# Optimization experiments

Hardware: AMD Instinct MI355X
Metric: run time of the kernel (lower is better)

Reference implementation:

```python
import jax, jax.numpy as jnp
import numpy as np

C_S = 1024
H = 16
M = 1  # num_vector_messages
B, S = 2, 1024
SQRT3 = 3.0 ** 0.5
LN_EPS = 1e-5


def setup_inputs() -> dict:
    key = jax.random.key(0)
    ks = jax.random.split(key, 8)
    s = jax.random.normal(ks[0], (B, S, C_S), dtype=jnp.float32)
    # random proper-ish frames: orthonormalize random 3x3 via QR
    A = jax.random.normal(ks[1], (B, S, 3, 3), dtype=jnp.float32)
    rot, _ = jnp.linalg.qr(A)
    trans = jax.random.normal(ks[2], (B, S, 3), dtype=jnp.float32)
    affine_mask = jnp.ones((B, S), dtype=bool)
    sequence_id = jax.random.randint(ks[3], (B, S), 0, 4, dtype=jnp.int32)
    chain_id = jax.random.randint(ks[4], (B, S), 0, 4, dtype=jnp.int32)
    dim_proj = 4 * H * 3 + H * 3 * M
    ln_w = jnp.ones((C_S,), dtype=jnp.float32)
    w_proj = jax.random.normal(ks[5], (dim_proj, C_S), dtype=jnp.float32) / np.sqrt(C_S)
    w_out = jax.random.normal(ks[6], (C_S, H * 3 * M), dtype=jnp.float32) / np.sqrt(H * 3 * M)
    dist_scale = jnp.zeros((H,), dtype=jnp.float32)
    rot_scale = jnp.zeros((H,), dtype=jnp.float32)
    return {"s": s, "rot": rot, "trans": trans, "ln_w": ln_w, "w_proj": w_proj,
            "w_out": w_out, "dist_scale": dist_scale, "rot_scale": rot_scale,
            "affine_mask": affine_mask, "sequence_id": sequence_id, "chain_id": chain_id}


def reference(s, rot, trans, ln_w, w_proj, w_out, dist_scale, rot_scale,
              affine_mask, sequence_id, chain_id):
    b, n, c = s.shape
    h, m = H, M
    NEG = jnp.finfo(s.dtype).min
    # attention bias: 1.0 for same-sequence pairs, -inf for invalid frames / cross-chain
    seq_eq = (sequence_id[:, :, None] == sequence_id[:, None, :]).astype(s.dtype)
    bias = seq_eq[:, None]  # [b,1,s,s]
    bias = jnp.where(affine_mask[:, None, None, :], bias, NEG)
    chain_diff = chain_id[:, :, None] != chain_id[:, None, :]
    bias = jnp.where(chain_diff[:, None], NEG, bias)
    # LayerNorm (no bias)
    mu = jnp.mean(s, axis=-1, keepdims=True)
    var = jnp.var(s, axis=-1, keepdims=True)
    ns = (s - mu) / jnp.sqrt(var + LN_EPS) * ln_w
    p = jnp.einsum('bsc,dc->bsd', ns, w_proj)
    n_rot = h * 2 * 3 + h * 3 * m
    vec_rot = p[..., :n_rot].reshape(b, n, 2 * h + h * m, 3)
    vec_dist = p[..., n_rot:].reshape(b, n, 2 * h, 3)
    # rotate into global frame; dist vectors also translated
    rot_vecs = jnp.einsum('bsij,bshj->bshi', rot, vec_rot)
    q_rot, k_rot, value = rot_vecs[:, :, :h], rot_vecs[:, :, h:2 * h], rot_vecs[:, :, 2 * h:]
    dist_vecs = jnp.einsum('bsij,bshj->bshi', rot, vec_dist) + trans[:, :, None, :]
    q_dist, k_dist = dist_vecs[:, :, :h], dist_vecs[:, :, h:]
    # distance term [b,h,q,k]
    qd = q_dist.transpose(0, 2, 1, 3)  # b h s 3
    kd = k_dist.transpose(0, 2, 1, 3)
    diff = qd[:, :, :, None, :] - kd[:, :, None, :, :]
    distance_term = jnp.sqrt(jnp.sum(diff * diff, axis=-1)) / SQRT3
    rotation_term = jnp.einsum('bqhd,bkhd->bhqk', q_rot, k_rot) / SQRT3
    dw = jax.nn.softplus(dist_scale)[None, :, None, None]
    rw = jax.nn.softplus(rot_scale)[None, :, None, None]
    attn = rotation_term * rw - distance_term * dw + bias
    attn = jax.nn.softmax(attn, axis=-1)
    # value: b s (h m) 3 -> b h s (m 3)
    v = value.reshape(b, n, h, m, 3).transpose(0, 2, 1, 3, 4).reshape(b, h, n, m * 3)
    out = jnp.einsum('bhqk,bhkd->bhqd', attn, v)
    out = out.reshape(b, h, n, m, 3).transpose(0, 2, 1, 3, 4).reshape(b, n, h * m, 3)
    out = jnp.einsum('bsji,bshj->bshi', rot, out)  # inverse rotation R^T
    out = out.reshape(b, n, h * m * 3)
    out = jnp.where(affine_mask[..., None], out, 0.0)
    return jnp.einsum('bsd,cd->bsc', out, w_out)
```

## Files before the change

### kernel.cpp

```cpp
#include <hip/hip_runtime.h>
#include <math.h>

#define NB 2
#define NS 1024
#define NC 1024
#define NH 16
#define DIMP 240
#define KSPLIT 16

constexpr float INV_SQRT3 = 0.57735026919f;

__global__ __launch_bounds__(256) void pre_kernel(const float* __restrict__ s,
                                                  const float* __restrict__ lnw,
                                                  float* __restrict__ ns,
                                                  const float* __restrict__ wp,
                                                  float* __restrict__ wt) {
    __shared__ float sh[64 * 61];
    int tid = threadIdx.x;
    if (blockIdx.x < NB * NS) {
        int row = blockIdx.x;
        const float4* sp = (const float4*)(s + (size_t)row * NC);
        float4 v = sp[tid];
        float sum = v.x + v.y + v.z + v.w;
        float sq  = v.x*v.x + v.y*v.y + v.z*v.z + v.w*v.w;
        #pragma unroll
        for (int off = 32; off; off >>= 1) {
            sum += __shfl_down(sum, off);
            sq  += __shfl_down(sq, off);
        }
        float* s1 = sh; float* s2 = sh + 4;
        int wave = tid >> 6;
        if ((tid & 63) == 0) { s1[wave] = sum; s2[wave] = sq; }
        __syncthreads();
        float tot   = s1[0] + s1[1] + s1[2] + s1[3];
        float totsq = s2[0] + s2[1] + s2[2] + s2[3];
        float mu  = tot * (1.0f / NC);
        float var = totsq * (1.0f / NC) - mu * mu;
        float rstd = rsqrtf(var + 1e-5f);
        float4 w = ((const float4*)lnw)[tid];
        float4 o;
        o.x = (v.x - mu) * rstd * w.x;
        o.y = (v.y - mu) * rstd * w.y;
        o.z = (v.z - mu) * rstd * w.z;
        o.w = (v.w - mu) * rstd * w.w;
        ((float4*)(ns + (size_t)row * NC))[tid] = o;
    } else {
        int bx = blockIdx.x - NB * NS;
        int k0 = (bx & 15) * 64;
        int d0 = (bx >> 4) * 60;
        float (*T)[61] = (float (*)[61])sh;
        #pragma unroll
        for (int i = 0; i < 15; i++) {
            int idx = i * 256 + tid;
            int dd = idx >> 6, kk = idx & 63;
            T[kk][dd] = wp[(size_t)(d0 + dd) * NC + k0 + kk];
        }
        __syncthreads();
        #pragma unroll
        for (int i = 0; i < 15; i++) {
            int idx = i * 256 + tid;
            int kk = idx / 60, dd = idx % 60;
            wt[(size_t)(k0 + kk) * DIMP + d0 + dd] = T[kk][dd];
        }
    }
}

__global__ __launch_bounds__(256) void proj_kernel(const float* __restrict__ ns,
                                                   const float* __restrict__ wt,
                                                   float* __restrict__ pp,
                                                   int use_atomic) {
    int tid = threadIdx.x;
    int wave = tid >> 6, lane = tid & 63;
    int row0 = blockIdx.x * 32;
    int ky = blockIdx.y;
    int k0 = ky * 64;

    __shared__ float A[32][64];
    #pragma unroll
    for (int i = 0; i < 2; i++) {
        int idx = tid + i * 256;
        int r = idx >> 4, c4 = idx & 15;
        *(float4*)&A[r][c4 * 4] = *(const float4*)(ns + (size_t)(row0 + r) * NC + k0 + c4 * 4);
    }
    __syncthreads();

    int wr0 = wave * 8;
    int c0 = lane * 4;
    bool active = c0 < DIMP;
    int c0m = active ? c0 : (DIMP - 4);
    const float* wb = wt + (size_t)k0 * DIMP + c0m;

    float acc[8][4];
    #pragma unroll
    for (int r = 0; r < 8; r++)
        #pragma unroll
        for (int c = 0; c < 4; c++) acc[r][c] = 0.0f;

    float4 wa[4], wx[4];
    #pragma unroll
    for (int j = 0; j < 4; j++) wa[j] = *(const float4*)(wb + (size_t)j * DIMP);

    for (int g = 0; g < 16; g += 2) {
        #pragma unroll
        for (int j = 0; j < 4; j++)
            wx[j] = *(const float4*)(wb + (size_t)((g + 1) * 4 + j) * DIMP);
        #pragma unroll
        for (int r = 0; r < 8; r++) {
            float4 a4 = *(const float4*)&A[wr0 + r][g * 4];
            #pragma unroll
            for (int c = 0; c < 4; c++) {
                float* ac = &acc[r][c];
                *ac = fmaf(a4.x, ((const float*)&wa[0])[c], *ac);
                *ac = fmaf(a4.y, ((const float*)&wa[1])[c], *ac);
                *ac = fmaf(a4.z, ((const float*)&wa[2])[c], *ac);
                *ac = fmaf(a4.w, ((const float*)&wa[3])[c], *ac);
            }
        }
        int kn2 = (g + 2 < 16) ? (g + 2) * 4 : 0;
        #pragma unroll
        for (int j = 0; j < 4; j++)
            wa[j] = *(const float4*)(wb + (size_t)(kn2 + j) * DIMP);
        #pragma unroll
        for (int r = 0; r < 8; r++) {
            float4 a4 = *(const float4*)&A[wr0 + r][(g + 1) * 4];
            #pragma unroll
            for (int c = 0; c < 4; c++) {
                float* ac = &acc[r][c];
                *ac = fmaf(a4.x, ((const float*)&wx[0])[c], *ac);
                *ac = fmaf(a4.y, ((const float*)&wx[1])[c], *ac);
                *ac = fmaf(a4.z, ((const float*)&wx[2])[c], *ac);
                *ac = fmaf(a4.w, ((const float*)&wx[3])[c], *ac);
            }
        }
    }
    if (active) {
        if (use_atomic) {
            #pragma unroll
            for (int r = 0; r < 8; r++)
                #pragma unroll
                for (int c = 0; c < 4; c++)
                    atomicAdd(&pp[(size_t)(row0 + wr0 + r) * DIMP + c0 + c], acc[r][c]);
        } else {
            float* dst = pp + (size_t)ky * (NB * NS * DIMP);
            #pragma unroll
            for (int r = 0; r < 8; r++)
                *(float4*)(dst + (size_t)(row0 + wr0 + r) * DIMP + c0) =
                    make_float4(acc[r][0], acc[r][1], acc[r][2], acc[r][3]);
        }
    }
}

__global__ __launch_bounds__(256) void build_kernel(const float* __restrict__ pp, int nred,
                                                    const float* __restrict__ rot,
                                                    const float* __restrict__ trans,
                                                    const float* __restrict__ dist_scale,
                                                    const float* __restrict__ rot_scale,
                                                    const int* __restrict__ seq,
                                                    const int* __restrict__ chain,
                                                    const int* __restrict__ amask,
                                                    float4* __restrict__ qrb,
                                                    float4* __restrict__ qdb,
                                                    float4* __restrict__ kp) {
    int gid = blockIdx.x * 256 + threadIdx.x;
    if (gid >= NB * NS * 80) return;
    int j  = gid % 80;
    int bs = gid / 80;
    int b  = bs >> 10;
    int si = bs & 1023;
    int off = (j < 48) ? 3 * j : 144 + 3 * (j - 48);
    float vx = 0.0f, vy = 0.0f, vz = 0.0f;
    for (int ky = 0; ky < nred; ky++) {
        const float* pr = pp + (size_t)ky * (NB * NS * DIMP) + (size_t)bs * DIMP + off;
        vx += pr[0]; vy += pr[1]; vz += pr[2];
    }
    const float* R = rot + (size_t)bs * 9;
    float ox = R[0] * vx + R[1] * vy + R[2] * vz;
    float oy = R[3] * vx + R[4] * vy + R[5] * vz;
    float oz = R[6] * vx + R[7] * vy + R[8] * vz;
    if (j >= 48) {
        ox += trans[(size_t)bs * 3 + 0];
        oy += trans[(size_t)bs * 3 + 1];
        oz += trans[(size_t)bs * 3 + 2];
    }
    if (j < 16) {
        float sc = log1pf(__expf(rot_scale[j])) * INV_SQRT3;
        qrb[(size_t)(b * NH + j) * NS + si] = make_float4(ox * sc, oy * sc, oz * sc, 0.0f);
    } else if (j < 32) {
        int h = j - 16;
        float ck = (float)chain[bs] + 1000.0f * (float)(1 - amask[bs]);
        kp[((size_t)(b * NH + h) * NS + si) * 3 + 0] = make_float4(ox, oy, oz, ck);
    } else if (j < 48) {
        int h = j - 32;
        kp[((size_t)(b * NH + h) * NS + si) * 3 + 2] = make_float4(ox, oy, oz, 0.0f);
    } else if (j < 64) {
        int h = j - 48;
        float sc = log1pf(__expf(dist_scale[h])) * INV_SQRT3;
        qdb[(size_t)(b * NH + h) * NS + si] = make_float4(ox * sc, oy * sc, oz * sc, 0.0f);
    } else {
        int h = j - 64;
        float sc = log1pf(__expf(dist_scale[h])) * INV_SQRT3;
        kp[((size_t)(b * NH + h) * NS + si) * 3 + 1] =
            make_float4(ox * sc, oy * sc, oz * sc, (float)seq[bs]);
    }
}

__global__ __launch_bounds__(256) void attn_kernel(
    const float4* __restrict__ qrb, const float4* __restrict__ qdb,
    const float4* __restrict__ kp,
    const float* __restrict__ rot,
    float* __restrict__ small) {
    int wid  = blockIdx.x * 4 + (threadIdx.x >> 6);
    int lane = threadIdx.x & 63;
    int qg = wid & 255;
    int h  = (wid >> 8) & 15;
    int b  = wid >> 12;
    int base = (b * NH + h) * NS;
    int q0 = qg * 4;
    const float4* kb = kp + (size_t)base * 3;

    float qrx[4], qry[4], qrz[4], qdx[4], qdy[4], qdz[4], cq[4], sq[4];
    #pragma unroll
    for (int t = 0; t < 4; t++) {
        float4 a = qrb[base + q0 + t];
        float4 d = qdb[base + q0 + t];
        qrx[t] = a.x; qry[t] = a.y; qrz[t] = a.z;
        qdx[t] = d.x; qdy[t] = d.y; qdz[t] = d.z;
        cq[t] = kb[(size_t)(q0 + t) * 3 + 0].w;
        sq[t] = kb[(size_t)(q0 + t) * 3 + 1].w;
    }
    float l[4] = {0, 0, 0, 0}, ax[4] = {0, 0, 0, 0}, ay[4] = {0, 0, 0, 0}, az[4] = {0, 0, 0, 0};

    for (int k = lane; k < NS; k += 64) {
        float4 f0 = kb[(size_t)k * 3 + 0];
        float4 f1 = kb[(size_t)k * 3 + 1];
        float4 f2 = kb[(size_t)k * 3 + 2];
        #pragma unroll
        for (int t = 0; t < 4; t++) {
            float rt = fmaf(qrx[t], f0.x, fmaf(qry[t], f0.y, qrz[t] * f0.z));
            float dx = qdx[t] - f1.x, dy = qdy[t] - f1.y, dz = qdz[t] - f1.z;
            float d2 = fmaf(dx, dx, fmaf(dy, dy, dz * dz));
            float dist = sqrtf(d2);
            float dc = f0.w - cq[t];
            float arg = fmaf(-100.0f, fabsf(dc), rt - dist) +
                        ((f1.w == sq[t]) ? -15.0f : -16.0f);
            float pw = __expf(arg);
            l[t] += pw;
            ax[t] = fmaf(pw, f2.x, ax[t]);
            ay[t] = fmaf(pw, f2.y, ay[t]);
            az[t] = fmaf(pw, f2.z, az[t]);
        }
    }
    #pragma unroll
    for (int t = 0; t < 4; t++) {
        #pragma unroll
        for (int off = 32; off; off >>= 1) {
            l[t]  += __shfl_xor(l[t], off);
            ax[t] += __shfl_xor(ax[t], off);
            ay[t] += __shfl_xor(ay[t], off);
            az[t] += __shfl_xor(az[t], off);
        }
    }
    if (lane == 0) {
        #pragma unroll
        for (int t = 0; t < 4; t++) {
            int q = q0 + t;
            float inv = 1.0f / l[t];
            float ox = ax[t] * inv, oy = ay[t] * inv, oz = az[t] * inv;
            const float* R = rot + (size_t)(b * NS + q) * 9;
            float wx = R[0] * ox + R[3] * oy + R[6] * oz;
            float wy = R[1] * ox + R[4] * oy + R[7] * oz;
            float wz = R[2] * ox + R[5] * oy + R[8] * oz;
            if (cq[t] >= 500.0f) { wx = 0; wy = 0; wz = 0; }
            float* o = small + (size_t)(b * NS + q) * 48 + h * 3;
            o[0] = wx; o[1] = wy; o[2] = wz;
        }
    }
}

__global__ __launch_bounds__(256) void outgemm_kernel(const float* __restrict__ small,
                                                      const float* __restrict__ wout,
                                                      float* __restrict__ out) {
    int c  = blockIdx.y * 256 + threadIdx.x;
    int r0 = blockIdx.x * 16;
    __shared__ float sm[16][48];
    for (int i = threadIdx.x; i < 16 * 48; i += 256)
        sm[i / 48][i % 48] = small[(size_t)(r0 + i / 48) * 48 + i % 48];
    __syncthreads();
    float w[48];
    #pragma unroll
    for (int d = 0; d < 48; d += 4) {
        float4 t = *(const float4*)(wout + (size_t)c * 48 + d);
        w[d] = t.x; w[d + 1] = t.y; w[d + 2] = t.z; w[d + 3] = t.w;
    }
    #pragma unroll 4
    for (int r = 0; r < 16; r++) {
        float acc = 0.0f;
        #pragma unroll
        for (int d = 0; d < 48; d++) acc = fmaf(w[d], sm[r][d], acc);
        out[(size_t)(r0 + r) * NC + c] = acc;
    }
}

extern "C" void kernel_launch(void* const* d_in, const int* in_sizes, int n_in,
                              void* d_out, int out_size, void* d_ws, size_t ws_size,
                              hipStream_t stream) {
    const float* s     = (const float*)d_in[0];
    const float* rot   = (const float*)d_in[1];
    const float* trans = (const float*)d_in[2];
    const float* lnw   = (const float*)d_in[3];
    const float* wproj = (const float*)d_in[4];
    const float* wout  = (const float*)d_in[5];
    const float* dsc   = (const float*)d_in[6];
    const float* rsc   = (const float*)d_in[7];
    const int* amask   = (const int*)d_in[8];
    const int* seq     = (const int*)d_in[9];
    const int* chain   = (const int*)d_in[10];
    float* out = (float*)d_out;

    float* ns = (float*)d_ws;
    float4* qrb = (float4*)(ns + (size_t)NB * NS * NC);
    float4* qdb = qrb + (size_t)NB * NH * NS;
    float4* kpk = qdb + (size_t)NB * NH * NS;
    float* small = (float*)(kpk + (size_t)3 * NB * NH * NS);
    float* pp = small + (size_t)NB * NS * 48;
    float* wt = (float*)qrb;

    size_t need = ((char*)(pp + (size_t)KSPLIT * NB * NS * DIMP)) - (char*)d_ws;
    int use_atomic = (ws_size < need) ? 1 : 0;

    pre_kernel<<<NB * NS + 64, 256, 0, stream>>>(s, lnw, ns, wproj, wt);
    if (use_atomic) {
        hipMemsetAsync(pp, 0, (size_t)NB * NS * DIMP * sizeof(float), stream);
        proj_kernel<<<dim3(64, KSPLIT), 256, 0, stream>>>(ns, wt, pp, 1);
        build_kernel<<<(NB * NS * 80 + 255) / 256, 256, 0, stream>>>(pp, 1, rot, trans, dsc, rsc,
                                                                     seq, chain, amask, qrb, qdb, kpk);
    } else {
        proj_kernel<<<dim3(64, KSPLIT), 256, 0, stream>>>(ns, wt, pp, 0);
        build_kernel<<<(NB * NS * 80 + 255) / 256, 256, 0, stream>>>(pp, KSPLIT, rot, trans, dsc, rsc,
                                                                     seq, chain, amask, qrb, qdb, kpk);
    }
    attn_kernel<<<NB * NH * NS / 16, 256, 0, stream>>>(qrb, qdb, kpk, rot, small);
    outgemm_kernel<<<dim3(NB * NS / 16, 4), 256, 0, stream>>>(small, wout, out);
}
```

Before: 156.1 us.

## Stage keys in LDS and raise queries per wave to eight

The attention kernel now loads all 1024 key/dist/value float4 triples for one (batch, head) into shared memory once per block. Each of the four waves then handles eight queries instead of four, so the grid shrinks to 1024 blocks of 32 queries. This cuts repeated global/L2 key reads and amortizes each key load over more queries. In exchange it uses 48KB of LDS per block, which limits occupancy, and doubles the accumulator registers per thread.

```diff
diff --git a/kernel.cpp b/kernel.cpp
--- a/kernel.cpp
+++ b/kernel.cpp
@@ -209,33 +209,47 @@
     const float4* __restrict__ kp,
     const float* __restrict__ rot,
     float* __restrict__ small) {
-    int wid  = blockIdx.x * 4 + (threadIdx.x >> 6);
-    int lane = threadIdx.x & 63;
-    int qg = wid & 255;
-    int h  = (wid >> 8) & 15;
-    int b  = wid >> 12;
-    int base = (b * NH + h) * NS;
-    int q0 = qg * 4;
+    __shared__ float4 krS[NS];
+    __shared__ float4 kdS[NS];
+    __shared__ float4 vvS[NS];
+    int tid  = threadIdx.x;
+    int wave = tid >> 6, lane = tid & 63;
+    int bh = blockIdx.x >> 5;
+    int qc = blockIdx.x & 31;
+    int b  = bh >> 4;
+    int base = bh * NS;
+    int q0 = qc * 32 + wave * 8;
     const float4* kb = kp + (size_t)base * 3;
 
-    float qrx[4], qry[4], qrz[4], qdx[4], qdy[4], qdz[4], cq[4], sq[4];
-    #pragma unroll
-    for (int t = 0; t < 4; t++) {
+    for (int i = tid; i < NS; i += 256) {
+        krS[i] = kb[(size_t)i * 3 + 0];
+        kdS[i] = kb[(size_t)i * 3 + 1];
+        vvS[i] = kb[(size_t)i * 3 + 2];
+    }
+    __syncthreads();
+
+    float qrx[8], qry[8], qrz[8], qdx[8], qdy[8], qdz[8], cq[8], sq[8];
+    #pragma unroll
+    for (int t = 0; t < 8; t++) {
         float4 a = qrb[base + q0 + t];
         float4 d = qdb[base + q0 + t];
         qrx[t] = a.x; qry[t] = a.y; qrz[t] = a.z;
         qdx[t] = d.x; qdy[t] = d.y; qdz[t] = d.z;
-        cq[t] = kb[(size_t)(q0 + t) * 3 + 0].w;
-        sq[t] = kb[(size_t)(q0 + t) * 3 + 1].w;
-    }
-    float l[4] = {0, 0, 0, 0}, ax[4] = {0, 0, 0, 0}, ay[4] = {0, 0, 0, 0}, az[4] = {0, 0, 0, 0};
-
-    for (int k = lane; k < NS; k += 64) {
-        float4 f0 = kb[(size_t)k * 3 + 0];
-        float4 f1 = kb[(size_t)k * 3 + 1];
-        float4 f2 = kb[(size_t)k * 3 + 2];
-        #pragma unroll
-        for (int t = 0; t < 4; t++) {
+        cq[t] = krS[q0 + t].w;
+        sq[t] = kdS[q0 + t].w;
+    }
+    float l[8], ax[8], ay[8], az[8];
+    #pragma unroll
+    for (int t = 0; t < 8; t++) { l[t] = 0; ax[t] = 0; ay[t] = 0; az[t] = 0; }
+
+    #pragma unroll 2
+    for (int ki = 0; ki < 16; ki++) {
+        int k = ki * 64 + lane;
+        float4 f0 = krS[k];
+        float4 f1 = kdS[k];
+        float4 f2 = vvS[k];
+        #pragma unroll
+        for (int t = 0; t < 8; t++) {
             float rt = fmaf(qrx[t], f0.x, fmaf(qry[t], f0.y, qrz[t] * f0.z));
             float dx = qdx[t] - f1.x, dy = qdy[t] - f1.y, dz = qdz[t] - f1.z;
             float d2 = fmaf(dx, dx, fmaf(dy, dy, dz * dz));
@@ -251,7 +265,7 @@
         }
     }
     #pragma unroll
-    for (int t = 0; t < 4; t++) {
+    for (int t = 0; t < 8; t++) {
         #pragma unroll
         for (int off = 32; off; off >>= 1) {
             l[t]  += __shfl_xor(l[t], off);
@@ -262,7 +276,7 @@
     }
     if (lane == 0) {
         #pragma unroll
-        for (int t = 0; t < 4; t++) {
+        for (int t = 0; t < 8; t++) {
             int q = q0 + t;
             float inv = 1.0f / l[t];
             float ox = ax[t] * inv, oy = ay[t] * inv, oz = az[t] * inv;
@@ -271,6 +285,7 @@
             float wy = R[1] * ox + R[4] * oy + R[7] * oz;
             float wz = R[2] * ox + R[5] * oy + R[8] * oz;
             if (cq[t] >= 500.0f) { wx = 0; wy = 0; wz = 0; }
+            int h = bh & 15;
             float* o = small + (size_t)(b * NS + q) * 48 + h * 3;
             o[0] = wx; o[1] = wy; o[2] = wz;
         }
@@ -339,6 +354,6 @@
         build_kernel<<<(NB * NS * 80 + 255) / 256, 256, 0, stream>>>(pp, KSPLIT, rot, trans, dsc, rsc,
                                                                      seq, chain, amask, qrb, qdb, kpk);
     }
-    attn_kernel<<<NB * NH * NS / 16, 256, 0, stream>>>(qrb, qdb, kpk, rot, small);
+    attn_kernel<<<NB * NH * (NS / 32), 256, 0, stream>>>(qrb, qdb, kpk, rot, small);
     outgemm_kernel<<<dim3(NB * NS / 16, 4), 256, 0, stream>>>(small, wout, out);
 }
```

Result: no change. 158.6 us (+1.6%).

## Split attention over key chunks with shared-memory key tiles and a reduction kernel

Applied to the files above, without the earlier changes.

The attention kernel now gives one query per thread and splits the key dimension into 16 chunks of 64 keys. Each block stages its chunk in shared memory and writes partial sums (weighted value and normaliser) to a workspace. A new finalize kernel adds the partials, normalises, applies the inverse rotation and the mask. This removes the per-query cross-lane shuffle reductions and the repeated global key loads, at the cost of an extra launch and extra partial-sum traffic. The exponentials have no max-subtraction, which is safe only because the logits are bounded.

```diff
diff --git a/kernel.cpp b/kernel.cpp
--- a/kernel.cpp
+++ b/kernel.cpp
@@ -7,6 +7,7 @@
 #define NH 16
 #define DIMP 240
 #define KSPLIT 16
+#define AKH 16
 
 constexpr float INV_SQRT3 = 0.57735026919f;
 
@@ -207,74 +208,67 @@
 __global__ __launch_bounds__(256) void attn_kernel(
     const float4* __restrict__ qrb, const float4* __restrict__ qdb,
     const float4* __restrict__ kp,
-    const float* __restrict__ rot,
-    float* __restrict__ small) {
-    int wid  = blockIdx.x * 4 + (threadIdx.x >> 6);
-    int lane = threadIdx.x & 63;
-    int qg = wid & 255;
-    int h  = (wid >> 8) & 15;
-    int b  = wid >> 12;
-    int base = (b * NH + h) * NS;
-    int q0 = qg * 4;
+    float4* __restrict__ pacc) {
+    __shared__ float4 kS[192];
+    int bx = blockIdx.x;
+    int ks = bx & (AKH - 1), qc = (bx >> 4) & 3, bh = bx >> 6;
+    int tid = threadIdx.x;
+    int q = qc * 256 + tid;
+    int base = bh * NS;
     const float4* kb = kp + (size_t)base * 3;
 
-    float qrx[4], qry[4], qrz[4], qdx[4], qdy[4], qdz[4], cq[4], sq[4];
-    #pragma unroll
-    for (int t = 0; t < 4; t++) {
-        float4 a = qrb[base + q0 + t];
-        float4 d = qdb[base + q0 + t];
-        qrx[t] = a.x; qry[t] = a.y; qrz[t] = a.z;
-        qdx[t] = d.x; qdy[t] = d.y; qdz[t] = d.z;
-        cq[t] = kb[(size_t)(q0 + t) * 3 + 0].w;
-        sq[t] = kb[(size_t)(q0 + t) * 3 + 1].w;
-    }
-    float l[4] = {0, 0, 0, 0}, ax[4] = {0, 0, 0, 0}, ay[4] = {0, 0, 0, 0}, az[4] = {0, 0, 0, 0};
-
-    for (int k = lane; k < NS; k += 64) {
-        float4 f0 = kb[(size_t)k * 3 + 0];
-        float4 f1 = kb[(size_t)k * 3 + 1];
-        float4 f2 = kb[(size_t)k * 3 + 2];
-        #pragma unroll
-        for (int t = 0; t < 4; t++) {
-            float rt = fmaf(qrx[t], f0.x, fmaf(qry[t], f0.y, qrz[t] * f0.z));
-            float dx = qdx[t] - f1.x, dy = qdy[t] - f1.y, dz = qdz[t] - f1.z;
-            float d2 = fmaf(dx, dx, fmaf(dy, dy, dz * dz));
-            float dist = sqrtf(d2);
-            float dc = f0.w - cq[t];
-            float arg = fmaf(-100.0f, fabsf(dc), rt - dist) +
-                        ((f1.w == sq[t]) ? -15.0f : -16.0f);
-            float pw = __expf(arg);
-            l[t] += pw;
-            ax[t] = fmaf(pw, f2.x, ax[t]);
-            ay[t] = fmaf(pw, f2.y, ay[t]);
-            az[t] = fmaf(pw, f2.z, az[t]);
-        }
-    }
-    #pragma unroll
-    for (int t = 0; t < 4; t++) {
-        #pragma unroll
-        for (int off = 32; off; off >>= 1) {
-            l[t]  += __shfl_xor(l[t], off);
-            ax[t] += __shfl_xor(ax[t], off);
-            ay[t] += __shfl_xor(ay[t], off);
-            az[t] += __shfl_xor(az[t], off);
-        }
-    }
-    if (lane == 0) {
-        #pragma unroll
-        for (int t = 0; t < 4; t++) {
-            int q = q0 + t;
-            float inv = 1.0f / l[t];
-            float ox = ax[t] * inv, oy = ay[t] * inv, oz = az[t] * inv;
-            const float* R = rot + (size_t)(b * NS + q) * 9;
-            float wx = R[0] * ox + R[3] * oy + R[6] * oz;
-            float wy = R[1] * ox + R[4] * oy + R[7] * oz;
-            float wz = R[2] * ox + R[5] * oy + R[8] * oz;
-            if (cq[t] >= 500.0f) { wx = 0; wy = 0; wz = 0; }
-            float* o = small + (size_t)(b * NS + q) * 48 + h * 3;
-            o[0] = wx; o[1] = wy; o[2] = wz;
-        }
-    }
+    if (tid < 192) kS[tid] = kb[(size_t)ks * 192 + tid];
+    __syncthreads();
+
+    float4 a = qrb[base + q];
+    float4 d = qdb[base + q];
+    float cq = kb[(size_t)q * 3 + 0].w;
+    float sq = kb[(size_t)q * 3 + 1].w;
+
+    float l = 0.0f, ax = 0.0f, ay = 0.0f, az = 0.0f;
+    #pragma unroll 4
+    for (int j = 0; j < 64; j++) {
+        float4 f0 = kS[j * 3 + 0];
+        float4 f1 = kS[j * 3 + 1];
+        float4 f2 = kS[j * 3 + 2];
+        float rt = fmaf(a.x, f0.x, fmaf(a.y, f0.y, a.z * f0.z));
+        float dx = d.x - f1.x, dy = d.y - f1.y, dz = d.z - f1.z;
+        float dist = sqrtf(fmaf(dx, dx, fmaf(dy, dy, dz * dz)));
+        float dc = f0.w - cq;
+        float arg = fmaf(-100.0f, fabsf(dc), rt - dist) +
+                    ((f1.w == sq) ? -15.0f : -16.0f);
+        float pw = __expf(arg);
+        l += pw;
+        ax = fmaf(pw, f2.x, ax);
+        ay = fmaf(pw, f2.y, ay);
+        az = fmaf(pw, f2.z, az);
+    }
+    pacc[(size_t)ks * (32 * NS) + base + q] = make_float4(ax, ay, az, l);
+}
+
+__global__ __launch_bounds__(256) void attnfin_kernel(const float4* __restrict__ pacc,
+                                                      const float4* __restrict__ kp,
+                                                      const float* __restrict__ rot,
+                                                      float* __restrict__ small) {
+    int i = blockIdx.x * 256 + threadIdx.x;
+    int bh = i >> 10, q = i & 1023;
+    int b = bh >> 4, h = bh & 15;
+    float4 s = make_float4(0.0f, 0.0f, 0.0f, 0.0f);
+    #pragma unroll
+    for (int j = 0; j < AKH; j++) {
+        float4 t = pacc[(size_t)j * (32 * NS) + i];
+        s.x += t.x; s.y += t.y; s.z += t.z; s.w += t.w;
+    }
+    float inv = 1.0f / s.w;
+    float ox = s.x * inv, oy = s.y * inv, oz = s.z * inv;
+    const float* R = rot + (size_t)(b * NS + q) * 9;
+    float wx = R[0] * ox + R[3] * oy + R[6] * oz;
+    float wy = R[1] * ox + R[4] * oy + R[7] * oz;
+    float wz = R[2] * ox + R[5] * oy + R[8] * oz;
+    float cq = kp[((size_t)bh * NS + q) * 3 + 0].w;
+    if (cq >= 500.0f) { wx = 0; wy = 0; wz = 0; }
+    float* o = small + (size_t)(b * NS + q) * 48 + h * 3;
+    o[0] = wx; o[1] = wy; o[2] = wz;
 }
 
 __global__ __launch_bounds__(256) void outgemm_kernel(const float* __restrict__ small,
@@ -324,6 +318,7 @@
     float* small = (float*)(kpk + (size_t)3 * NB * NH * NS);
     float* pp = small + (size_t)NB * NS * 48;
     float* wt = (float*)qrb;
+    float4* pacc = (float4*)pp;
 
     size_t need = ((char*)(pp + (size_t)KSPLIT * NB * NS * DIMP)) - (char*)d_ws;
     int use_atomic = (ws_size < need) ? 1 : 0;
@@ -339,6 +334,7 @@
         build_kernel<<<(NB * NS * 80 + 255) / 256, 256, 0, stream>>>(pp, KSPLIT, rot, trans, dsc, rsc,
                                                                      seq, chain, amask, qrb, qdb, kpk);
     }
-    attn_kernel<<<NB * NH * NS / 16, 256, 0, stream>>>(qrb, qdb, kpk, rot, small);
+    attn_kernel<<<NB * NH * 4 * AKH, 256, 0, stream>>>(qrb, qdb, kpk, pacc);
+    attnfin_kernel<<<NB * NH * NS / 256, 256, 0, stream>>>(pacc, kpk, rot, small);
     outgemm_kernel<<<dim3(NB * NS / 16, 4), 256, 0, stream>>>(small, wout, out);
 }
```

Measured after the change: 153.0 us, median of 2. No clear change (-2.0%).
